# Kernel optimization log

Hardware: AMD Instinct MI355X
Metric: run time of the kernel (lower is better)

## Reference

```python
import jax, jax.numpy as jnp
import numpy as np

N_ITEMS = 200000
EMB = 100
LAYERS = 3
N_EDGES = 6400000


def setup_inputs() -> dict:
    key = jax.random.key(0)
    k1, k2, k3, k4, k5 = jax.random.split(key, 5)
    embedding = jax.random.normal(k1, (N_ITEMS, EMB), dtype=jnp.float32)
    adj_vals = jax.random.uniform(k2, (N_EDGES,), dtype=jnp.float32)
    weights = jax.random.normal(k3, (LAYERS, EMB, EMB), dtype=jnp.float32) * (1.0 / np.sqrt(EMB))
    adj_rows = jax.random.randint(k4, (N_EDGES,), 0, N_ITEMS, dtype=jnp.int32)
    adj_cols = jax.random.randint(k5, (N_EDGES,), 0, N_ITEMS, dtype=jnp.int32)
    return {"embedding": embedding, "adj_vals": adj_vals, "weights": weights,
            "adj_rows": adj_rows, "adj_cols": adj_cols}


def reference(embedding, adj_vals, weights, adj_rows, adj_cols):
    # embedding: [N, d]; weights: [L, d, d] (torch Linear weight, y = x @ W.T)
    # adjacency in COO: out[r] += v * x[c]
    n = embedding.shape[0]
    eps = 1e-12  # F.normalize eps
    x = embedding
    finals = [x]  # layer-0 copy is NOT normalized (matches original)
    for i in range(weights.shape[0]):
        x = jnp.einsum('nd,ed->ne', x, weights[i])          # linear, no bias
        gathered = adj_vals[:, None] * x[adj_cols]           # [E, d]
        x = jax.ops.segment_sum(gathered, adj_rows, num_segments=n)  # SpMM
        norm = jnp.maximum(jnp.linalg.norm(x, axis=-1, keepdims=True), eps)
        finals.append(x / norm)  # appended copy normalized; carried x stays raw
    return jnp.mean(jnp.stack(finals, axis=0), axis=0)
```

## Files before the change

### kernel.cpp

```cpp
#include <hip/hip_runtime.h>

#define EMB 100
#define EMB2 50
#define XSTRIDE 52
#define Y8DW 32
#define BSHIFT 8
#define BROWS 256
#define MAXBUCK 1024
#define CHUNK 32768

typedef __attribute__((ext_vector_type(8))) short short8;
typedef __attribute__((ext_vector_type(4))) float f32x4;
typedef __attribute__((ext_vector_type(2))) float f2v;

__device__ __forceinline__ unsigned packbf(float a, float b) {
    unsigned ua = __float_as_uint(a), ub = __float_as_uint(b);
    unsigned ra = (ua + 0x7FFFu + ((ua >> 16) & 1u)) >> 16;
    unsigned rb = (ub + 0x7FFFu + ((ub >> 16) & 1u)) >> 16;
    return ra | (rb << 16);
}

__device__ __forceinline__ unsigned char f32_to_fp8(float f) {
    unsigned u = __float_as_uint(f);
    unsigned s = (u >> 24) & 0x80u;
    unsigned mag = u & 0x7FFFFFFFu;
    if (mag >= 0x43E00000u) return (unsigned char)(s | 0x7Eu);
    if (mag < 0x3C800000u) {
        int r = __float2int_rn(__uint_as_float(mag) * 512.f);
        return (unsigned char)(s | (unsigned)r);
    }
    unsigned r = mag + 0x7FFFFu + ((mag >> 20) & 1u);
    unsigned e = r >> 23, m = (r >> 20) & 7u;
    return (unsigned char)(s | ((e - 120u) << 3) | m);
}

__device__ __forceinline__ unsigned pack4_fp8(float a0, float a1, float a2, float a3) {
#if __has_builtin(__builtin_amdgcn_cvt_pk_fp8_f32)
    int lo = __builtin_amdgcn_cvt_pk_fp8_f32(a0, a1, 0, false);
    return (unsigned)__builtin_amdgcn_cvt_pk_fp8_f32(a2, a3, lo, true);
#else
    return (unsigned)f32_to_fp8(a0) | ((unsigned)f32_to_fp8(a1) << 8) |
           ((unsigned)f32_to_fp8(a2) << 16) | ((unsigned)f32_to_fp8(a3) << 24);
#endif
}

__device__ __forceinline__ void fma_fp8x4(unsigned g, float v,
                                          float& a0, float& a1, float& a2, float& a3) {
#if __has_builtin(__builtin_amdgcn_cvt_pk_f32_fp8)
    f2v lo = __builtin_amdgcn_cvt_pk_f32_fp8((int)g, false);
    f2v hi = __builtin_amdgcn_cvt_pk_f32_fp8((int)g, true);
    a0 = fmaf(v, lo[0], a0); a1 = fmaf(v, lo[1], a1);
    a2 = fmaf(v, hi[0], a2); a3 = fmaf(v, hi[1], a3);
#else
    float o[4];
#pragma unroll
    for (int d = 0; d < 4; ++d) {
        unsigned b = (g >> (8 * d)) & 0xFFu;
        unsigned e = (b >> 3) & 15u, m = b & 7u;
        float val = e ? __uint_as_float(((e + 120u) << 23) | (m << 20))
                      : (float)m * (1.f / 512.f);
        o[d] = (b & 0x80u) ? -val : val;
    }
    a0 = fmaf(v, o[0], a0); a1 = fmaf(v, o[1], a1);
    a2 = fmaf(v, o[2], a2); a3 = fmaf(v, o[3], a3);
#endif
}

__global__ __launch_bounds__(256) void k_bucket_count(const int* __restrict__ rows,
                                                      int* __restrict__ gcnt,
                                                      int E, int nbuck) {
    __shared__ int hist[MAXBUCK];
    int tid = threadIdx.x;
    int base = blockIdx.x * CHUNK;
    for (int s = tid; s < nbuck; s += 256) hist[s] = 0;
    __syncthreads();
#pragma unroll 4
    for (int k = 0; k < CHUNK / 256; ++k) {
        int i = base + tid + k * 256;
        if (i < E) atomicAdd(&hist[rows[i] >> BSHIFT], 1);
    }
    __syncthreads();
    for (int s = tid; s < nbuck; s += 256)
        if (hist[s]) atomicAdd(&gcnt[s], hist[s]);
}

__global__ __launch_bounds__(1024) void k_scan2(int* __restrict__ bsum, int nb) {
    __shared__ int tmp[1024];
    int v = (threadIdx.x < nb) ? bsum[threadIdx.x] : 0;
    tmp[threadIdx.x] = v;
    __syncthreads();
    for (int off = 1; off < 1024; off <<= 1) {
        int t = (threadIdx.x >= off) ? tmp[threadIdx.x - off] : 0;
        __syncthreads();
        tmp[threadIdx.x] += t;
        __syncthreads();
    }
    if (threadIdx.x < nb) bsum[threadIdx.x] = tmp[threadIdx.x] - v;
}

__global__ __launch_bounds__(256) void k_partition(const int* __restrict__ rows,
                                                   const int* __restrict__ cols,
                                                   const float* __restrict__ vals,
                                                   int* __restrict__ bucket_next,
                                                   int2* __restrict__ part,
                                                   int E, int nbuck) {
    __shared__ int hist[MAXBUCK];
    __shared__ int base_s[MAXBUCK];
    __shared__ int cnt2[MAXBUCK];
    int tid = threadIdx.x;
    int base = blockIdx.x * CHUNK;
    for (int s = tid; s < nbuck; s += 256) hist[s] = 0;
    __syncthreads();
#pragma unroll 4
    for (int k = 0; k < CHUNK / 256; ++k) {
        int i = base + tid + k * 256;
        if (i < E) atomicAdd(&hist[rows[i] >> BSHIFT], 1);
    }
    __syncthreads();
    for (int s = tid; s < nbuck; s += 256) {
        if (hist[s]) base_s[s] = atomicAdd(&bucket_next[s], hist[s]);
        cnt2[s] = 0;
    }
    __syncthreads();
#pragma unroll 4
    for (int k = 0; k < CHUNK / 256; ++k) {
        int i = base + tid + k * 256;
        if (i < E) {
            int r = rows[i];
            int b = r >> BSHIFT;
            unsigned q = (unsigned)__float2int_rn(vals[i] * 16383.f);
            unsigned cv = (unsigned)cols[i] | (q << 18);
            int rank = atomicAdd(&cnt2[b], 1);
            part[base_s[b] + rank] = make_int2(r, (int)cv);
        }
    }
}

__global__ __launch_bounds__(256) void k_build_csr(const int2* __restrict__ part,
                                                   const int* __restrict__ bucket_end,
                                                   int* __restrict__ row_ptr,
                                                   unsigned* __restrict__ csr,
                                                   int N, int E) {
    __shared__ int cnt[BROWS];
    __shared__ int scn[BROWS];
    __shared__ int cur[BROWS];
    int b = blockIdx.x;
    int tid = threadIdx.x;
    int seg_beg = (b == 0) ? 0 : bucket_end[b - 1];
    int seg_end = bucket_end[b];
    int rowbase = b << BSHIFT;

    cnt[tid] = 0;
    __syncthreads();
    for (int i = seg_beg + tid; i < seg_end; i += 256)
        atomicAdd(&cnt[part[i].x - rowbase], 1);
    __syncthreads();
    int v = cnt[tid];
    scn[tid] = v;
    __syncthreads();
    for (int off = 1; off < 256; off <<= 1) {
        int t = (tid >= off) ? scn[tid - off] : 0;
        __syncthreads();
        scn[tid] += t;
        __syncthreads();
    }
    int rp = seg_beg + scn[tid] - v;
    if (rowbase + tid < N) row_ptr[rowbase + tid] = rp;
    cur[tid] = rp;
    if (b == 0 && tid == 0) row_ptr[N] = E;
    __syncthreads();
    for (int i = seg_beg + tid; i < seg_end; i += 256) {
        int2 e = part[i];
        int pos = atomicAdd(&cur[e.x - rowbase], 1);
        csr[pos] = (unsigned)e.y;
    }
}

template <bool F32SRC>
__global__ __launch_bounds__(256) void k_gemm_mfma(const void* __restrict__ Xv,
                                                   const float* __restrict__ W,
                                                   unsigned* __restrict__ Y8,
                                                   int nTiles, int N) {
    __shared__ uint4 Bf[28][64];
    int tid = threadIdx.x;
#pragma unroll
    for (int it = 0; it < 7; ++it) {
        int id = it * 256 + tid;
        int fs = id >> 6, lane = id & 63;
        int nt = fs >> 2, ks = fs & 3;
        int e = nt * 16 + (lane & 15);
        int dbase = ks * 32 + (lane >> 4) * 8;
        float w[8];
#pragma unroll
        for (int j = 0; j < 8; ++j) {
            int d = dbase + j;
            w[j] = (e < EMB && d < EMB) ? W[e * EMB + d] : 0.f;
        }
        uint4 u;
        u.x = packbf(w[0], w[1]); u.y = packbf(w[2], w[3]);
        u.z = packbf(w[4], w[5]); u.w = packbf(w[6], w[7]);
        Bf[fs][lane] = u;
    }
    __syncthreads();

    int wid = (blockIdx.x * 256 + tid) >> 6;
    int nWaves = gridDim.x * 4;
    int lane = tid & 63;
    int m = lane & 15, kg = lane >> 4;

    for (int tile = wid; tile < nTiles; tile += nWaves) {
        int rowbase = tile * 16;
        int arow = rowbase + m; if (arow >= N) arow = N - 1;
        uint4 a[4];
        if (F32SRC) {
            const float* xr = (const float*)Xv + (size_t)arow * EMB;
#pragma unroll
            for (int ks = 0; ks < 3; ++ks) {
                float4 v0 = *(const float4*)(xr + ks * 32 + kg * 8);
                float4 v1 = *(const float4*)(xr + ks * 32 + kg * 8 + 4);
                a[ks] = make_uint4(packbf(v0.x, v0.y), packbf(v0.z, v0.w),
                                   packbf(v1.x, v1.y), packbf(v1.z, v1.w));
            }
            uint4 t = make_uint4(0, 0, 0, 0);
            if (kg == 0) { float4 v = *(const float4*)(xr + 96);
                           t.x = packbf(v.x, v.y); t.y = packbf(v.z, v.w); }
            a[3] = t;
        } else {
            const unsigned* xr = (const unsigned*)Xv + (size_t)arow * XSTRIDE;
#pragma unroll
            for (int ks = 0; ks < 3; ++ks)
                a[ks] = *(const uint4*)(xr + ks * 16 + kg * 4);
            uint4 t = make_uint4(0, 0, 0, 0);
            if (kg == 0) { uint2 v = *(const uint2*)(xr + 48); t.x = v.x; t.y = v.y; }
            a[3] = t;
        }

        f32x4 acc[7];
#pragma unroll
        for (int nt = 0; nt < 7; ++nt) acc[nt] = (f32x4){0.f, 0.f, 0.f, 0.f};
#pragma unroll
        for (int ks = 0; ks < 4; ++ks) {
            short8 av = __builtin_bit_cast(short8, a[ks]);
#pragma unroll
            for (int nt = 0; nt < 7; ++nt) {
                short8 bv = __builtin_bit_cast(short8, Bf[nt * 4 + ks][lane]);
                acc[nt] = __builtin_amdgcn_mfma_f32_16x16x32_bf16(bv, av, acc[nt], 0, 0, 0);
            }
        }
        int rr = rowbase + m;
        if (rr < N) {
            unsigned* yrow = Y8 + ((size_t)rr << 5) + kg;
#pragma unroll
            for (int nt = 0; nt < 6; ++nt)
                yrow[nt * 4] = pack4_fp8(acc[nt][0], acc[nt][1], acc[nt][2], acc[nt][3]);
            if (kg == 0)
                yrow[24] = pack4_fp8(acc[6][0], acc[6][1], acc[6][2], acc[6][3]);
        }
    }
}

__global__ __launch_bounds__(256) void k_spmm_norm(const int* __restrict__ row_ptr,
                                                   const unsigned* __restrict__ csr,
                                                   const unsigned* __restrict__ Y8,
                                                   unsigned* __restrict__ Xout,
                                                   float* __restrict__ Out,
                                                   const float* __restrict__ prev,
                                                   float pscale, float scale,
                                                   int writeX, int N) {
    int wave = (blockIdx.x * 256 + threadIdx.x) >> 6;
    int lane = threadIdx.x & 63;
    if (wave >= N) return;
    int half = lane >> 5, sub = lane & 31;
    int beg = row_ptr[wave], end = row_ptr[wave + 1];
    const float dq = 1.0f / 16383.f;
    float a0 = 0.f, a1 = 0.f, a2 = 0.f, a3 = 0.f;
    if (sub < 25) {
        const unsigned* yb = Y8 + sub;
        int j = beg + half;
        for (; j + 14 < end; j += 16) {
            unsigned u[8], g[8];
#pragma unroll
            for (int t = 0; t < 8; ++t)
                u[t] = __builtin_nontemporal_load(&csr[j + 2 * t]);
#pragma unroll
            for (int t = 0; t < 8; ++t)
                g[t] = yb[(u[t] & 0x3FFFFu) << 5];
#pragma unroll
            for (int t = 0; t < 8; ++t)
                fma_fp8x4(g[t], (float)(u[t] >> 18) * dq, a0, a1, a2, a3);
        }
        for (; j + 6 < end; j += 8) {
            unsigned u[4], g[4];
#pragma unroll
            for (int t = 0; t < 4; ++t)
                u[t] = __builtin_nontemporal_load(&csr[j + 2 * t]);
#pragma unroll
            for (int t = 0; t < 4; ++t)
                g[t] = yb[(u[t] & 0x3FFFFu) << 5];
#pragma unroll
            for (int t = 0; t < 4; ++t)
                fma_fp8x4(g[t], (float)(u[t] >> 18) * dq, a0, a1, a2, a3);
        }
        for (; j < end; j += 2) {
            unsigned u = csr[j];
            unsigned g = yb[(u & 0x3FFFFu) << 5];
            fma_fp8x4(g, (float)(u >> 18) * dq, a0, a1, a2, a3);
        }
    }
    a0 += __shfl_xor(a0, 32, 64);
    a1 += __shfl_xor(a1, 32, 64);
    a2 += __shfl_xor(a2, 32, 64);
    a3 += __shfl_xor(a3, 32, 64);
    float ss = fmaf(a0, a0, fmaf(a1, a1, fmaf(a2, a2, a3 * a3)));
#pragma unroll
    for (int off = 16; off; off >>= 1) ss += __shfl_xor(ss, off, 64);
    float sc = scale / fmaxf(sqrtf(ss), 1e-12f);
    if (half == 0 && sub < 25) {
        if (writeX) {
            uint2 xw;
            xw.x = packbf(a0, a1); xw.y = packbf(a2, a3);
            *(uint2*)(Xout + (size_t)wave * XSTRIDE + sub * 2) = xw;
        }
        const float4* pp = (const float4*)(prev + (size_t)wave * EMB) + sub;
        float4 p = *pp;
        float4 o;
        o.x = fmaf(a0, sc, p.x * pscale);
        o.y = fmaf(a1, sc, p.y * pscale);
        o.z = fmaf(a2, sc, p.z * pscale);
        o.w = fmaf(a3, sc, p.w * pscale);
        *((float4*)(Out + (size_t)wave * EMB) + sub) = o;
    }
}

extern "C" void kernel_launch(void* const* d_in, const int* in_sizes, int n_in,
                              void* d_out, int out_size, void* d_ws, size_t ws_size,
                              hipStream_t stream) {
    const float* emb   = (const float*)d_in[0];
    const float* avals = (const float*)d_in[1];
    const float* wts   = (const float*)d_in[2];
    const int*   arows = (const int*)d_in[3];
    const int*   acols = (const int*)d_in[4];

    const int N = in_sizes[0] / EMB;
    const int E = in_sizes[1];
    const int L = in_sizes[2] / (EMB * EMB);
    const float scale = 1.0f / (float)(L + 1);
    const int nbuck = (N + BROWS - 1) >> BSHIFT;

    unsigned* Y8     = (unsigned*)d_ws;
    unsigned* bufX   = Y8 + (size_t)N * Y8DW;
    int* row_ptr     = (int*)(bufX + (size_t)N * XSTRIDE);
    int* bucket_next = row_ptr + (N + 2);
    unsigned* csr    = (unsigned*)(bucket_next + MAXBUCK);
    int2* part       = (int2*)d_ws;
    float* out = (float*)d_out;

    const int nchunk = (E + CHUNK - 1) / CHUNK;

    hipMemsetAsync(bucket_next, 0, MAXBUCK * sizeof(int), stream);
    k_bucket_count<<<nchunk, 256, 0, stream>>>(arows, bucket_next, E, nbuck);
    k_scan2<<<1, 1024, 0, stream>>>(bucket_next, nbuck);
    k_partition<<<nchunk, 256, 0, stream>>>(arows, acols, avals, bucket_next,
                                            part, E, nbuck);
    k_build_csr<<<nbuck, 256, 0, stream>>>(part, bucket_next, row_ptr, csr, N, E);

    const int nTiles = (N + 15) / 16;
    const int gemm_blocks = 782;
    const int spmm_blocks = (N + 3) / 4;

    k_gemm_mfma<true><<<gemm_blocks, 256, 0, stream>>>(emb, wts, Y8, nTiles, N);
    k_spmm_norm<<<spmm_blocks, 256, 0, stream>>>(row_ptr, csr, Y8, bufX,
                                                 out, emb, scale, scale, 1, N);
    for (int l = 1; l < L; ++l) {
        k_gemm_mfma<false><<<gemm_blocks, 256, 0, stream>>>(
            bufX, wts + (size_t)l * EMB * EMB, Y8, nTiles, N);
        k_spmm_norm<<<spmm_blocks, 256, 0, stream>>>(row_ptr, csr, Y8, bufX,
                                                     out, out, 1.0f, scale,
                                                     (l < L - 1) ? 1 : 0, N);
    }
}
```

Baseline: 904.0 us.

## Stage partition through LDS and widen SpMM gathers to 8-byte per-lane loads

The partition kernel now uses smaller chunks, keeps edges in registers, computes local bucket offsets with a block scan, and stages sorted edges in LDS. This lets the global scatter to the partition buffer be written in contiguous runs instead of random atomic-ranked stores. The SpMM kernel is restructured so that four 16-lane groups each gather a whole 128-byte fp8 row with uint2 loads, instead of 25 lanes doing 4-byte loads over two halves. Because of that, the padding dword of each Y8 row is now zeroed. The new SpMM loop has no unrolled prefetch batches and handles the tail with masked loads, which may reduce memory-level parallelism per wave.

```diff
diff --git a/kernel.cpp b/kernel.cpp
--- a/kernel.cpp
+++ b/kernel.cpp
@@ -1,13 +1,13 @@
 #include <hip/hip_runtime.h>
 
 #define EMB 100
-#define EMB2 50
 #define XSTRIDE 52
 #define Y8DW 32
 #define BSHIFT 8
 #define BROWS 256
 #define MAXBUCK 1024
-#define CHUNK 32768
+#define CHUNK 4096
+#define EPT (CHUNK / 256)
 
 typedef __attribute__((ext_vector_type(8))) short short8;
 typedef __attribute__((ext_vector_type(4))) float f32x4;
@@ -74,8 +74,8 @@
     int base = blockIdx.x * CHUNK;
     for (int s = tid; s < nbuck; s += 256) hist[s] = 0;
     __syncthreads();
-#pragma unroll 4
-    for (int k = 0; k < CHUNK / 256; ++k) {
+#pragma unroll
+    for (int k = 0; k < EPT; ++k) {
         int i = base + tid + k * 256;
         if (i < E) atomicAdd(&hist[rows[i] >> BSHIFT], 1);
     }
@@ -105,34 +105,70 @@
                                                    int2* __restrict__ part,
                                                    int E, int nbuck) {
     __shared__ int hist[MAXBUCK];
+    __shared__ int loc[MAXBUCK];
     __shared__ int base_s[MAXBUCK];
-    __shared__ int cnt2[MAXBUCK];
+    __shared__ int scan256[256];
+    __shared__ int2 stage[CHUNK];
     int tid = threadIdx.x;
     int base = blockIdx.x * CHUNK;
+    int nE = E - base; if (nE > CHUNK) nE = CHUNK;
+
     for (int s = tid; s < nbuck; s += 256) hist[s] = 0;
     __syncthreads();
-#pragma unroll 4
-    for (int k = 0; k < CHUNK / 256; ++k) {
-        int i = base + tid + k * 256;
-        if (i < E) atomicAdd(&hist[rows[i] >> BSHIFT], 1);
-    }
-    __syncthreads();
-    for (int s = tid; s < nbuck; s += 256) {
-        if (hist[s]) base_s[s] = atomicAdd(&bucket_next[s], hist[s]);
-        cnt2[s] = 0;
-    }
-    __syncthreads();
-#pragma unroll 4
-    for (int k = 0; k < CHUNK / 256; ++k) {
-        int i = base + tid + k * 256;
-        if (i < E) {
+
+    int r_[EPT]; unsigned cv_[EPT];
+#pragma unroll
+    for (int k = 0; k < EPT; ++k) {
+        int o = tid + k * 256;
+        if (o < nE) {
+            int i = base + o;
             int r = rows[i];
-            int b = r >> BSHIFT;
             unsigned q = (unsigned)__float2int_rn(vals[i] * 16383.f);
-            unsigned cv = (unsigned)cols[i] | (q << 18);
-            int rank = atomicAdd(&cnt2[b], 1);
-            part[base_s[b] + rank] = make_int2(r, (int)cv);
-        }
+            r_[k] = r;
+            cv_[k] = (unsigned)cols[i] | (q << 18);
+            atomicAdd(&hist[r >> BSHIFT], 1);
+        } else { r_[k] = -1; cv_[k] = 0; }
+    }
+    __syncthreads();
+
+    for (int s = tid; s < nbuck; s += 256)
+        base_s[s] = hist[s] ? atomicAdd(&bucket_next[s], hist[s]) : 0;
+
+    int s4 = tid * 4;
+    int h0 = (s4     < nbuck) ? hist[s4]     : 0;
+    int h1 = (s4 + 1 < nbuck) ? hist[s4 + 1] : 0;
+    int h2 = (s4 + 2 < nbuck) ? hist[s4 + 2] : 0;
+    int h3 = (s4 + 3 < nbuck) ? hist[s4 + 3] : 0;
+    int tot = h0 + h1 + h2 + h3;
+    scan256[tid] = tot;
+    __syncthreads();
+    for (int off = 1; off < 256; off <<= 1) {
+        int t = (tid >= off) ? scan256[tid - off] : 0;
+        __syncthreads();
+        scan256[tid] += t;
+        __syncthreads();
+    }
+    int excl = scan256[tid] - tot;
+    if (s4     < nbuck) { loc[s4]     = excl;                hist[s4]     = 0; }
+    if (s4 + 1 < nbuck) { loc[s4 + 1] = excl + h0;           hist[s4 + 1] = 0; }
+    if (s4 + 2 < nbuck) { loc[s4 + 2] = excl + h0 + h1;      hist[s4 + 2] = 0; }
+    if (s4 + 3 < nbuck) { loc[s4 + 3] = excl + h0 + h1 + h2; hist[s4 + 3] = 0; }
+    __syncthreads();
+
+#pragma unroll
+    for (int k = 0; k < EPT; ++k) {
+        if (r_[k] >= 0) {
+            int b = r_[k] >> BSHIFT;
+            int rank = atomicAdd(&hist[b], 1);
+            stage[loc[b] + rank] = make_int2(r_[k], (int)cv_[k]);
+        }
+    }
+    __syncthreads();
+
+    for (int k = tid; k < nE; k += 256) {
+        int2 e = stage[k];
+        int b = e.x >> BSHIFT;
+        part[base_s[b] + (k - loc[b])] = e;
     }
 }
 
@@ -255,6 +291,8 @@
                 yrow[nt * 4] = pack4_fp8(acc[nt][0], acc[nt][1], acc[nt][2], acc[nt][3]);
             if (kg == 0)
                 yrow[24] = pack4_fp8(acc[6][0], acc[6][1], acc[6][2], acc[6][3]);
+            if (kg == 1)
+                yrow[24] = 0;
         }
     }
 }
@@ -270,65 +308,76 @@
     int wave = (blockIdx.x * 256 + threadIdx.x) >> 6;
     int lane = threadIdx.x & 63;
     if (wave >= N) return;
-    int half = lane >> 5, sub = lane & 31;
+    int g = lane >> 4, lg = lane & 15;
     int beg = row_ptr[wave], end = row_ptr[wave + 1];
     const float dq = 1.0f / 16383.f;
     float a0 = 0.f, a1 = 0.f, a2 = 0.f, a3 = 0.f;
-    if (sub < 25) {
-        const unsigned* yb = Y8 + sub;
-        int j = beg + half;
-        for (; j + 14 < end; j += 16) {
-            unsigned u[8], g[8];
-#pragma unroll
-            for (int t = 0; t < 8; ++t)
-                u[t] = __builtin_nontemporal_load(&csr[j + 2 * t]);
-#pragma unroll
-            for (int t = 0; t < 8; ++t)
-                g[t] = yb[(u[t] & 0x3FFFFu) << 5];
-#pragma unroll
-            for (int t = 0; t < 8; ++t)
-                fma_fp8x4(g[t], (float)(u[t] >> 18) * dq, a0, a1, a2, a3);
-        }
-        for (; j + 6 < end; j += 8) {
-            unsigned u[4], g[4];
-#pragma unroll
-            for (int t = 0; t < 4; ++t)
-                u[t] = __builtin_nontemporal_load(&csr[j + 2 * t]);
-#pragma unroll
-            for (int t = 0; t < 4; ++t)
-                g[t] = yb[(u[t] & 0x3FFFFu) << 5];
-#pragma unroll
-            for (int t = 0; t < 4; ++t)
-                fma_fp8x4(g[t], (float)(u[t] >> 18) * dq, a0, a1, a2, a3);
-        }
-        for (; j < end; j += 2) {
-            unsigned u = csr[j];
-            unsigned g = yb[(u & 0x3FFFFu) << 5];
-            fma_fp8x4(g, (float)(u >> 18) * dq, a0, a1, a2, a3);
-        }
-    }
-    a0 += __shfl_xor(a0, 32, 64);
-    a1 += __shfl_xor(a1, 32, 64);
-    a2 += __shfl_xor(a2, 32, 64);
-    a3 += __shfl_xor(a3, 32, 64);
-    float ss = fmaf(a0, a0, fmaf(a1, a1, fmaf(a2, a2, a3 * a3)));
-#pragma unroll
-    for (int off = 16; off; off >>= 1) ss += __shfl_xor(ss, off, 64);
+    float a4 = 0.f, a5 = 0.f, a6 = 0.f, a7 = 0.f;
+    const unsigned char* Yb = (const unsigned char*)Y8;
+
+    if (beg < end) {
+        for (int j4 = beg; j4 < end; j4 += 32) {
+#pragma unroll
+            for (int t = 0; t < 8; ++t) {
+                int je = j4 + t * 4 + g;
+                bool ok = je < end;
+                unsigned u = __builtin_nontemporal_load(&csr[ok ? je : beg]);
+                float v = ok ? (float)(u >> 18) * dq : 0.f;
+                uint2 gg = *(const uint2*)(Yb + ((size_t)(u & 0x3FFFFu) << 7) + lg * 8);
+                fma_fp8x4(gg.x, v, a0, a1, a2, a3);
+                fma_fp8x4(gg.y, v, a4, a5, a6, a7);
+            }
+        }
+    }
+    a0 += __shfl_xor(a0, 16, 64); a0 += __shfl_xor(a0, 32, 64);
+    a1 += __shfl_xor(a1, 16, 64); a1 += __shfl_xor(a1, 32, 64);
+    a2 += __shfl_xor(a2, 16, 64); a2 += __shfl_xor(a2, 32, 64);
+    a3 += __shfl_xor(a3, 16, 64); a3 += __shfl_xor(a3, 32, 64);
+    a4 += __shfl_xor(a4, 16, 64); a4 += __shfl_xor(a4, 32, 64);
+    a5 += __shfl_xor(a5, 16, 64); a5 += __shfl_xor(a5, 32, 64);
+    a6 += __shfl_xor(a6, 16, 64); a6 += __shfl_xor(a6, 32, 64);
+    a7 += __shfl_xor(a7, 16, 64); a7 += __shfl_xor(a7, 32, 64);
+
+    float ss = 0.f;
+    if (lg < 13) {
+        ss = a0 * a0 + a1 * a1 + a2 * a2 + a3 * a3 +
+             a4 * a4 + a5 * a5 + a6 * a6 + a7 * a7;
+    }
+#pragma unroll
+    for (int off = 1; off < 16; off <<= 1) ss += __shfl_xor(ss, off, 64);
     float sc = scale / fmaxf(sqrtf(ss), 1e-12f);
-    if (half == 0 && sub < 25) {
+
+    if (lane < 13) {
         if (writeX) {
-            uint2 xw;
-            xw.x = packbf(a0, a1); xw.y = packbf(a2, a3);
-            *(uint2*)(Xout + (size_t)wave * XSTRIDE + sub * 2) = xw;
-        }
-        const float4* pp = (const float4*)(prev + (size_t)wave * EMB) + sub;
-        float4 p = *pp;
-        float4 o;
-        o.x = fmaf(a0, sc, p.x * pscale);
-        o.y = fmaf(a1, sc, p.y * pscale);
-        o.z = fmaf(a2, sc, p.z * pscale);
-        o.w = fmaf(a3, sc, p.w * pscale);
-        *((float4*)(Out + (size_t)wave * EMB) + sub) = o;
+            unsigned* xp = Xout + (size_t)wave * XSTRIDE + lane * 4;
+            if (lane < 12) {
+                uint4 xw;
+                xw.x = packbf(a0, a1); xw.y = packbf(a2, a3);
+                xw.z = packbf(a4, a5); xw.w = packbf(a6, a7);
+                *(uint4*)xp = xw;
+            } else {
+                uint2 xw; xw.x = packbf(a0, a1); xw.y = packbf(a2, a3);
+                *(uint2*)xp = xw;
+            }
+        }
+        const float* pr = prev + (size_t)wave * EMB + lane * 8;
+        float* op = Out + (size_t)wave * EMB + lane * 8;
+        float4 p0 = *(const float4*)pr;
+        float4 o0;
+        o0.x = fmaf(a0, sc, p0.x * pscale);
+        o0.y = fmaf(a1, sc, p0.y * pscale);
+        o0.z = fmaf(a2, sc, p0.z * pscale);
+        o0.w = fmaf(a3, sc, p0.w * pscale);
+        *(float4*)op = o0;
+        if (lane < 12) {
+            float4 p1 = *(const float4*)(pr + 4);
+            float4 o1;
+            o1.x = fmaf(a4, sc, p1.x * pscale);
+            o1.y = fmaf(a5, sc, p1.y * pscale);
+            o1.z = fmaf(a6, sc, p1.z * pscale);
+            o1.w = fmaf(a7, sc, p1.w * pscale);
+            *(float4*)(op + 4) = o1;
+        }
     }
 }
 
```

After: 788.2 us. 12.8% less time.
